# Kernel tuning notes

Hardware: AMD Instinct MI355X
Metric: run time of the kernel (lower is better)

## Reference

```python
import jax, jax.numpy as jnp
import numpy as np

BN_EPS = 1e-5


def setup_inputs() -> dict:
    key = jax.random.key(0)
    k1, k2, k3 = jax.random.split(key, 3)
    x = jax.random.normal(k1, (16, 256, 128, 128), dtype=jnp.float32)
    # Conv2d(2, 1, kernel_size=7, padding=3): weight [out=1, in=2, 7, 7], bias [1]
    fan_in = 2 * 7 * 7
    bound = 1.0 / np.sqrt(fan_in)
    conv_w = jax.random.uniform(k2, (1, 2, 7, 7), minval=-bound, maxval=bound, dtype=jnp.float32)
    conv_b = jax.random.uniform(k3, (1,), minval=-bound, maxval=bound, dtype=jnp.float32)
    # BatchNorm2d(1) params (inference mode with running stats)
    bn_gamma = jnp.ones((1,), dtype=jnp.float32)
    bn_beta = jnp.zeros((1,), dtype=jnp.float32)
    bn_mean = jnp.zeros((1,), dtype=jnp.float32)
    bn_var = jnp.ones((1,), dtype=jnp.float32)
    return {"x": x, "conv_w": conv_w, "conv_b": conv_b,
            "bn_gamma": bn_gamma, "bn_beta": bn_beta,
            "bn_mean": bn_mean, "bn_var": bn_var}


def reference(x, conv_w, conv_b, bn_gamma, bn_beta, bn_mean, bn_var):
    # ChannelPool: concat(max over C, mean over C) -> [B, 2, H, W]
    x_pool = jnp.stack([jnp.max(x, axis=1), jnp.mean(x, axis=1)], axis=1)
    # 7x7 conv, stride 1, padding 3: [B, 2, H, W] -> [B, 1, H, W]
    y = jax.lax.conv_general_dilated(
        x_pool, conv_w,
        window_strides=(1, 1), padding=((3, 3), (3, 3)),
        dimension_numbers=('NCHW', 'OIHW', 'NCHW'))
    y = y + conv_b[None, :, None, None]
    # BatchNorm2d(1), inference mode with running stats
    inv = jax.lax.rsqrt(bn_var + BN_EPS)
    y = (y - bn_mean[None, :, None, None]) * (bn_gamma * inv)[None, :, None, None] + bn_beta[None, :, None, None]
    # sigmoid gate, broadcast multiply over channels
    x_att = jax.nn.sigmoid(y)
    return x * x_att
```

## Files before the change

kernel.cpp:

```cpp
#include <hip/hip_runtime.h>

#define BB 16
#define CC 256
#define HH 128
#define WW 128
#define HWSZ (HH * WW)
#define HW4 (HWSZ / 4)
#define BHW (BB * HWSZ)
#define TOTAL (BB * CC * HWSZ)

typedef float f32x4 __attribute__((ext_vector_type(4)));

__global__ __launch_bounds__(256) void pool_kernel(const float* __restrict__ x,
                                                   float* __restrict__ pmax,
                                                   float* __restrict__ pmean) {
    __shared__ float4 smax[256];
    __shared__ float4 ssum[256];
    int t     = threadIdx.x;
    int pos   = t & 63;
    int chunk = t >> 6;
    int gpos  = blockIdx.x * 64 + pos;
    int b     = gpos >> 12;
    int hw4   = gpos & (HW4 - 1);
    const float4* xb = (const float4*)x + ((size_t)b << 20) + ((size_t)chunk << 18) + hw4;

    float4 v = xb[0];
    float mx0 = v.x, mx1 = v.y, mx2 = v.z, mx3 = v.w;
    float s0 = v.x, s1 = v.y, s2 = v.z, s3 = v.w;
    #pragma unroll 8
    for (int c = 1; c < 64; ++c) {
        float4 u = xb[(size_t)c << 12];
        mx0 = fmaxf(mx0, u.x); s0 += u.x;
        mx1 = fmaxf(mx1, u.y); s1 += u.y;
        mx2 = fmaxf(mx2, u.z); s2 += u.z;
        mx3 = fmaxf(mx3, u.w); s3 += u.w;
    }
    smax[t] = make_float4(mx0, mx1, mx2, mx3);
    ssum[t] = make_float4(s0, s1, s2, s3);
    __syncthreads();

    if (t < 64) {
        float4 m0 = smax[t],       m1 = smax[t + 64],
               m2 = smax[t + 128], m3 = smax[t + 192];
        float4 a0 = ssum[t],       a1 = ssum[t + 64],
               a2 = ssum[t + 128], a3 = ssum[t + 192];
        float4 m, a;
        m.x = fmaxf(fmaxf(m0.x, m1.x), fmaxf(m2.x, m3.x));
        m.y = fmaxf(fmaxf(m0.y, m1.y), fmaxf(m2.y, m3.y));
        m.z = fmaxf(fmaxf(m0.z, m1.z), fmaxf(m2.z, m3.z));
        m.w = fmaxf(fmaxf(m0.w, m1.w), fmaxf(m2.w, m3.w));
        const float inv = 1.0f / (float)CC;
        a.x = (a0.x + a1.x + a2.x + a3.x) * inv;
        a.y = (a0.y + a1.y + a2.y + a3.y) * inv;
        a.z = (a0.z + a1.z + a2.z + a3.z) * inv;
        a.w = (a0.w + a1.w + a2.w + a3.w) * inv;
        ((float4*)pmax)[gpos]  = m;
        ((float4*)pmean)[gpos] = a;
    }
}

__global__ __launch_bounds__(256) void conv_kernel(const float* __restrict__ pmax,
                                                   const float* __restrict__ pmean,
                                                   const float* __restrict__ cw,
                                                   const float* __restrict__ cb,
                                                   const float* __restrict__ g,
                                                   const float* __restrict__ be,
                                                   const float* __restrict__ mu,
                                                   const float* __restrict__ var,
                                                   float* __restrict__ att) {
    __shared__ float w[98];
    __shared__ float sc[2];
    if (threadIdx.x < 98) w[threadIdx.x] = cw[threadIdx.x];
    if (threadIdx.x == 0) {
        float scale = g[0] * rsqrtf(var[0] + 1e-5f);
        sc[0] = scale;
        sc[1] = cb[0] * scale + be[0] - mu[0] * scale;
    }
    __syncthreads();

    int s  = blockIdx.x * 256 + threadIdx.x;
    int b  = s >> 14;
    int hw = s & (HWSZ - 1);
    int h  = hw >> 7;
    int ww = hw & 127;
    const float* pm = pmax  + (size_t)b * HWSZ;
    const float* pa = pmean + (size_t)b * HWSZ;

    float acc = 0.0f;
    #pragma unroll
    for (int kh = 0; kh < 7; ++kh) {
        int hh = h + kh - 3;
        if ((unsigned)hh < (unsigned)HH) {
            int rowoff = hh << 7;
            #pragma unroll
            for (int kw = 0; kw < 7; ++kw) {
                int wcol = ww + kw - 3;
                if ((unsigned)wcol < (unsigned)WW) {
                    int o = rowoff + wcol;
                    acc = fmaf(w[kh * 7 + kw],      pm[o], acc);
                    acc = fmaf(w[49 + kh * 7 + kw], pa[o], acc);
                }
            }
        }
    }
    float y = fmaf(acc, sc[0], sc[1]);
    att[s] = 1.0f / (1.0f + __expf(-y));
}

__global__ __launch_bounds__(256) void mul_kernel(const float* __restrict__ x,
                                                  const float* __restrict__ att,
                                                  float* __restrict__ out,
                                                  int total4) {
    int stride = gridDim.x * 256;
    const f32x4* xv = (const f32x4*)x;
    f32x4*       ov = (f32x4*)out;
    for (int i = blockIdx.x * 256 + threadIdx.x; i < total4; i += stride) {
        int p   = i >> 12;
        int b   = p >> 8;
        int hw4 = i & (HW4 - 1);
        float4 a = ((const float4*)att)[(b << 12) + hw4];
        f32x4 v = xv[i];
        v.x *= a.x; v.y *= a.y; v.z *= a.z; v.w *= a.w;
        __builtin_nontemporal_store(v, ov + i);
    }
}

extern "C" void kernel_launch(void* const* d_in, const int* in_sizes, int n_in,
                              void* d_out, int out_size, void* d_ws, size_t ws_size,
                              hipStream_t stream) {
    const float* x   = (const float*)d_in[0];
    const float* cw  = (const float*)d_in[1];
    const float* cb  = (const float*)d_in[2];
    const float* g   = (const float*)d_in[3];
    const float* be  = (const float*)d_in[4];
    const float* mu  = (const float*)d_in[5];
    const float* var = (const float*)d_in[6];
    float* out = (float*)d_out;

    float* pmax  = (float*)d_ws;
    float* pmean = pmax + BHW;
    float* att   = pmean + BHW;

    pool_kernel<<<BHW / 4 / 64, 256, 0, stream>>>(x, pmax, pmean);
    conv_kernel<<<BHW / 256, 256, 0, stream>>>(pmax, pmean, cw, cb, g, be, mu, var, att);
    mul_kernel<<<4096, 256, 0, stream>>>(x, att, out, TOTAL / 4);
}
```

Measured before the change: 148.6 us.

## Fuse conv gate into multiply kernel with shared-memory halo tiles

Merges the 7x7 conv/sigmoid kernel and the broadcast multiply into one kernel. Each block loads an 8-row strip of pooled maps with halo into shared memory, computes the attention for 8x128 pixels, and then scales 32 channels of x. This removes the attention buffer round-trip and one launch, and the conv reads shared memory instead of global. In exchange, the conv for each strip is recomputed 8 times, once per channel split, and the multiply phase per block is now a short fixed loop rather than a grid-stride loop.

```diff
diff --git a/kernel.cpp b/kernel.cpp
--- a/kernel.cpp
+++ b/kernel.cpp
@@ -59,7 +59,8 @@
     }
 }
 
-__global__ __launch_bounds__(256) void conv_kernel(const float* __restrict__ pmax,
+__global__ __launch_bounds__(256) void gate_kernel(const float* __restrict__ x,
+                                                   const float* __restrict__ pmax,
                                                    const float* __restrict__ pmean,
                                                    const float* __restrict__ cw,
                                                    const float* __restrict__ cb,
@@ -67,61 +68,78 @@
                                                    const float* __restrict__ be,
                                                    const float* __restrict__ mu,
                                                    const float* __restrict__ var,
-                                                   float* __restrict__ att) {
-    __shared__ float w[98];
+                                                   float* __restrict__ out) {
+    __shared__ float spm[14][134];
+    __shared__ float spa[14][134];
+    __shared__ float satt[8][128];
+    __shared__ float wsm[98];
     __shared__ float sc[2];
-    if (threadIdx.x < 98) w[threadIdx.x] = cw[threadIdx.x];
-    if (threadIdx.x == 0) {
+
+    int t      = threadIdx.x;
+    int bid    = blockIdx.x;
+    int csplit = bid & 7;
+    int rowgrp = (bid >> 3) & 15;
+    int b      = bid >> 7;
+    int r0     = rowgrp << 3;
+
+    if (t < 98) wsm[t] = cw[t];
+    if (t == 0) {
         float scale = g[0] * rsqrtf(var[0] + 1e-5f);
         sc[0] = scale;
         sc[1] = cb[0] * scale + be[0] - mu[0] * scale;
     }
+
+    int pbase = b * HWSZ;
+    #pragma unroll
+    for (int r = 0; r < 14; ++r) {
+        if (t < 134) {
+            int gr = r0 + r - 3;
+            int gc = t - 3;
+            float vm = 0.0f, va = 0.0f;
+            if ((unsigned)gr < (unsigned)HH && (unsigned)gc < (unsigned)WW) {
+                int off = pbase + (gr << 7) + gc;
+                vm = pmax[off];
+                va = pmean[off];
+            }
+            spm[r][t] = vm;
+            spa[r][t] = va;
+        }
+    }
     __syncthreads();
 
-    int s  = blockIdx.x * 256 + threadIdx.x;
-    int b  = s >> 14;
-    int hw = s & (HWSZ - 1);
-    int h  = hw >> 7;
-    int ww = hw & 127;
-    const float* pm = pmax  + (size_t)b * HWSZ;
-    const float* pa = pmean + (size_t)b * HWSZ;
-
-    float acc = 0.0f;
     #pragma unroll
-    for (int kh = 0; kh < 7; ++kh) {
-        int hh = h + kh - 3;
-        if ((unsigned)hh < (unsigned)HH) {
-            int rowoff = hh << 7;
+    for (int k = 0; k < 4; ++k) {
+        int pos = t + (k << 8);
+        int r   = pos >> 7;
+        int c   = pos & 127;
+        float acc = 0.0f;
+        #pragma unroll
+        for (int kh = 0; kh < 7; ++kh) {
             #pragma unroll
             for (int kw = 0; kw < 7; ++kw) {
-                int wcol = ww + kw - 3;
-                if ((unsigned)wcol < (unsigned)WW) {
-                    int o = rowoff + wcol;
-                    acc = fmaf(w[kh * 7 + kw],      pm[o], acc);
-                    acc = fmaf(w[49 + kh * 7 + kw], pa[o], acc);
-                }
+                acc = fmaf(wsm[kh * 7 + kw],      spm[r + kh][c + kw], acc);
+                acc = fmaf(wsm[49 + kh * 7 + kw], spa[r + kh][c + kw], acc);
             }
         }
+        float y = fmaf(acc, sc[0], sc[1]);
+        satt[r][c] = 1.0f / (1.0f + __expf(-y));
     }
-    float y = fmaf(acc, sc[0], sc[1]);
-    att[s] = 1.0f / (1.0f + __expf(-y));
-}
+    __syncthreads();
 
-__global__ __launch_bounds__(256) void mul_kernel(const float* __restrict__ x,
-                                                  const float* __restrict__ att,
-                                                  float* __restrict__ out,
-                                                  int total4) {
-    int stride = gridDim.x * 256;
+    int row8 = t >> 5;
+    int col4 = t & 31;
+    int grow = r0 + row8;
+    f32x4 a = *(const f32x4*)&satt[row8][col4 << 2];
     const f32x4* xv = (const f32x4*)x;
     f32x4*       ov = (f32x4*)out;
-    for (int i = blockIdx.x * 256 + threadIdx.x; i < total4; i += stride) {
-        int p   = i >> 12;
-        int b   = p >> 8;
-        int hw4 = i & (HW4 - 1);
-        float4 a = ((const float4*)att)[(b << 12) + hw4];
-        f32x4 v = xv[i];
+    int c0 = csplit << 5;
+    int xi = (((b << 8) + c0) << 12) + (grow << 5) + col4;
+    #pragma unroll 4
+    for (int ch = 0; ch < 32; ++ch) {
+        f32x4 v = xv[xi];
         v.x *= a.x; v.y *= a.y; v.z *= a.z; v.w *= a.w;
-        __builtin_nontemporal_store(v, ov + i);
+        __builtin_nontemporal_store(v, ov + xi);
+        xi += HW4;
     }
 }
 
@@ -139,9 +157,7 @@
 
     float* pmax  = (float*)d_ws;
     float* pmean = pmax + BHW;
-    float* att   = pmean + BHW;
 
     pool_kernel<<<BHW / 4 / 64, 256, 0, stream>>>(x, pmax, pmean);
-    conv_kernel<<<BHW / 256, 256, 0, stream>>>(pmax, pmean, cw, cb, g, be, mu, var, att);
-    mul_kernel<<<4096, 256, 0, stream>>>(x, att, out, TOTAL / 4);
+    gate_kernel<<<BB * 16 * 8, 256, 0, stream>>>(x, pmax, pmean, cw, cb, g, be, mu, var, out);
 }
```

After: 137.6 us, median of 3. 7.4% less time.

## Widen pool blocks to two positions per thread; stage attention map in LDS for gating

Applied to the files above, without the earlier changes.

The pool kernel now has each thread reduce two float4 positions across its channel chunk, so blocks cover 128 positions and the grid shrinks from 1024 to 512 blocks. The gating multiply is rewritten so each block loads one batch's full 64KB attention map into shared memory, then streams 8 channels of x against it. This replaces repeated global attention reads with LDS reads. The cost is lower occupancy from the large LDS allocation and only 512 blocks for a bandwidth-bound stream.

```diff
diff --git a/kernel.cpp b/kernel.cpp
--- a/kernel.cpp
+++ b/kernel.cpp
@@ -14,36 +14,38 @@
 __global__ __launch_bounds__(256) void pool_kernel(const float* __restrict__ x,
                                                    float* __restrict__ pmax,
                                                    float* __restrict__ pmean) {
-    __shared__ float4 smax[256];
-    __shared__ float4 ssum[256];
+    __shared__ float4 smax[4][128];
+    __shared__ float4 ssum[4][128];
     int t     = threadIdx.x;
-    int pos   = t & 63;
+    int lane  = t & 63;
     int chunk = t >> 6;
-    int gpos  = blockIdx.x * 64 + pos;
-    int b     = gpos >> 12;
-    int hw4   = gpos & (HW4 - 1);
+    int p0    = blockIdx.x * 128 + lane;
+    int b     = p0 >> 12;
+    int hw4   = p0 & (HW4 - 1);
     const float4* xb = (const float4*)x + ((size_t)b << 20) + ((size_t)chunk << 18) + hw4;
 
-    float4 v = xb[0];
-    float mx0 = v.x, mx1 = v.y, mx2 = v.z, mx3 = v.w;
-    float s0 = v.x, s1 = v.y, s2 = v.z, s3 = v.w;
-    #pragma unroll 8
+    float4 v0 = xb[0], v1 = xb[64];
+    float4 mA = v0, sA = v0, mB = v1, sB = v1;
+    #pragma unroll 4
     for (int c = 1; c < 64; ++c) {
-        float4 u = xb[(size_t)c << 12];
-        mx0 = fmaxf(mx0, u.x); s0 += u.x;
-        mx1 = fmaxf(mx1, u.y); s1 += u.y;
-        mx2 = fmaxf(mx2, u.z); s2 += u.z;
-        mx3 = fmaxf(mx3, u.w); s3 += u.w;
+        float4 u0 = xb[(size_t)(c << 12)];
+        float4 u1 = xb[(size_t)(c << 12) + 64];
+        mA.x = fmaxf(mA.x, u0.x); sA.x += u0.x;
+        mA.y = fmaxf(mA.y, u0.y); sA.y += u0.y;
+        mA.z = fmaxf(mA.z, u0.z); sA.z += u0.z;
+        mA.w = fmaxf(mA.w, u0.w); sA.w += u0.w;
+        mB.x = fmaxf(mB.x, u1.x); sB.x += u1.x;
+        mB.y = fmaxf(mB.y, u1.y); sB.y += u1.y;
+        mB.z = fmaxf(mB.z, u1.z); sB.z += u1.z;
+        mB.w = fmaxf(mB.w, u1.w); sB.w += u1.w;
     }
-    smax[t] = make_float4(mx0, mx1, mx2, mx3);
-    ssum[t] = make_float4(s0, s1, s2, s3);
+    smax[chunk][lane]      = mA;  ssum[chunk][lane]      = sA;
+    smax[chunk][lane + 64] = mB;  ssum[chunk][lane + 64] = sB;
     __syncthreads();
 
-    if (t < 64) {
-        float4 m0 = smax[t],       m1 = smax[t + 64],
-               m2 = smax[t + 128], m3 = smax[t + 192];
-        float4 a0 = ssum[t],       a1 = ssum[t + 64],
-               a2 = ssum[t + 128], a3 = ssum[t + 192];
+    if (t < 128) {
+        float4 m0 = smax[0][t], m1 = smax[1][t], m2 = smax[2][t], m3 = smax[3][t];
+        float4 a0 = ssum[0][t], a1 = ssum[1][t], a2 = ssum[2][t], a3 = ssum[3][t];
         float4 m, a;
         m.x = fmaxf(fmaxf(m0.x, m1.x), fmaxf(m2.x, m3.x));
         m.y = fmaxf(fmaxf(m0.y, m1.y), fmaxf(m2.y, m3.y));
@@ -54,8 +56,9 @@
         a.y = (a0.y + a1.y + a2.y + a3.y) * inv;
         a.z = (a0.z + a1.z + a2.z + a3.z) * inv;
         a.w = (a0.w + a1.w + a2.w + a3.w) * inv;
-        ((float4*)pmax)[gpos]  = m;
-        ((float4*)pmean)[gpos] = a;
+        int gp = blockIdx.x * 128 + t;
+        ((float4*)pmax)[gp]  = m;
+        ((float4*)pmean)[gp] = a;
     }
 }
 
@@ -107,21 +110,34 @@
     att[s] = 1.0f / (1.0f + __expf(-y));
 }
 
-__global__ __launch_bounds__(256) void mul_kernel(const float* __restrict__ x,
-                                                  const float* __restrict__ att,
-                                                  float* __restrict__ out,
-                                                  int total4) {
-    int stride = gridDim.x * 256;
+__global__ __launch_bounds__(256) void gate_kernel(const float* __restrict__ x,
+                                                   const float* __restrict__ att,
+                                                   float* __restrict__ out) {
+    __shared__ f32x4 satt[HW4];
+    int t  = threadIdx.x;
+    int cg = blockIdx.x & 31;
+    int b  = blockIdx.x >> 5;
+
+    const f32x4* attv = (const f32x4*)att + ((size_t)b << 12);
+    #pragma unroll
+    for (int j = 0; j < 16; ++j)
+        satt[j * 256 + t] = attv[j * 256 + t];
+    __syncthreads();
+
     const f32x4* xv = (const f32x4*)x;
     f32x4*       ov = (f32x4*)out;
-    for (int i = blockIdx.x * 256 + threadIdx.x; i < total4; i += stride) {
-        int p   = i >> 12;
-        int b   = p >> 8;
-        int hw4 = i & (HW4 - 1);
-        float4 a = ((const float4*)att)[(b << 12) + hw4];
-        f32x4 v = xv[i];
-        v.x *= a.x; v.y *= a.y; v.z *= a.z; v.w *= a.w;
-        __builtin_nontemporal_store(v, ov + i);
+    size_t base = (((size_t)b << 8) + ((size_t)cg << 3)) << 12;
+    #pragma unroll
+    for (int p = 0; p < 8; ++p) {
+        size_t pb = base + ((size_t)p << 12);
+        #pragma unroll 8
+        for (int k = 0; k < 16; ++k) {
+            int o = k * 256 + t;
+            f32x4 v = xv[pb + o];
+            f32x4 a = satt[o];
+            v.x *= a.x; v.y *= a.y; v.z *= a.z; v.w *= a.w;
+            __builtin_nontemporal_store(v, ov + pb + o);
+        }
     }
 }
 
@@ -141,7 +157,7 @@
     float* pmean = pmax + BHW;
     float* att   = pmean + BHW;
 
-    pool_kernel<<<BHW / 4 / 64, 256, 0, stream>>>(x, pmax, pmean);
+    pool_kernel<<<512, 256, 0, stream>>>(x, pmax, pmean);
     conv_kernel<<<BHW / 256, 256, 0, stream>>>(pmax, pmean, cw, cb, g, be, mu, var, att);
-    mul_kernel<<<4096, 256, 0, stream>>>(x, att, out, TOTAL / 4);
+    gate_kernel<<<512, 256, 0, stream>>>(x, att, out);
 }
```

Measured after the change: 157.6 us. +6.1%, slower.
